# Performance work log

Measured on AMD Instinct MI355X. Metric: run time of the kernel, lower is better.

The kernel has to match this reference:

```python
import jax, jax.numpy as jnp
import numpy as np

N_HEADS = 8

def setup_inputs() -> dict:
    key = jax.random.key(0)
    k0, k1, k2, k3, k4 = jax.random.split(key, 5)
    B, S, D = 2, 2048, 1024
    scale = 0.02
    return {
        "x": jax.random.normal(k0, (B, S, D), dtype=jnp.float32),
        "Wk": jax.random.normal(k1, (D, D), dtype=jnp.float32) * scale,
        "Wv": jax.random.normal(k2, (D, D), dtype=jnp.float32) * scale,
        "Wself": jax.random.normal(k3, (D, D), dtype=jnp.float32) * scale,
        "Wout": jax.random.normal(k4, (D, D), dtype=jnp.float32) * scale,
    }

def reference(x, Wk, Wv, Wself, Wout):
    B, S, D = x.shape
    H = N_HEADS
    hd = D // H
    # torch Linear: y = x @ W.T (no bias)
    keys = (x @ Wk.T).reshape(B, S, H, hd).transpose(0, 2, 1, 3)  # [B,H,S,hd]
    vals = (x @ Wv.T).reshape(B, S, H, hd).transpose(0, 2, 1, 3)  # [B,H,S,hd]
    # energy = K K^T / sqrt(hd); weights = softmax(-energy) with causal mask
    neg_energy = -jnp.einsum("bhqd,bhkd->bhqk", keys, keys) / jnp.sqrt(
        jnp.asarray(hd, dtype=x.dtype))
    causal = jnp.tril(jnp.ones((S, S), dtype=bool))  # allowed positions
    neg_energy = jnp.where(causal, neg_energy, -jnp.inf)
    weights = jax.nn.softmax(neg_energy, axis=-1)  # [B,H,S,S]
    pairwise = jnp.einsum("bhqk,bhkd->bhqd", weights, vals)
    pairwise = pairwise.transpose(0, 2, 1, 3).reshape(B, S, D)
    self_force = x @ Wself.T
    return (pairwise + self_force) @ Wout.T
```

## Files before the change

### kernel.cpp

```cpp
#include <hip/hip_runtime.h>


typedef unsigned short u16;
typedef short s16x8 __attribute__((ext_vector_type(8)));
typedef short s16x4 __attribute__((ext_vector_type(4)));
typedef unsigned short u16x4 __attribute__((ext_vector_type(4)));
typedef unsigned short u16x8 __attribute__((ext_vector_type(8)));
typedef float f32x4 __attribute__((ext_vector_type(4)));

#define DEV __device__ __forceinline__

DEV u16 f2bf(float f) {
    union { float f; unsigned u; } v; v.f = f;
    return (u16)((v.u + 0x7FFFu + ((v.u >> 16) & 1u)) >> 16);
}
DEV float bf2f(u16 h) {
    union { unsigned u; float f; } v; v.u = ((unsigned)h) << 16;
    return v.f;
}
DEV void gload16(const void* g, void* l) {
    __builtin_amdgcn_global_load_lds(
        (const __attribute__((address_space(1))) void*)g,
        (__attribute__((address_space(3))) void*)l, 16, 0, 0);
}

#define FULL_BARRIER()                          \
    do {                                        \
        __builtin_amdgcn_sched_barrier(0);      \
        __builtin_amdgcn_s_barrier();           \
        __builtin_amdgcn_sched_barrier(0);      \
    } while (0)

__global__ __launch_bounds__(256) void cast_all(
    const float* __restrict__ x, const float* __restrict__ wk,
    const float* __restrict__ wv, const float* __restrict__ wsf,
    const float* __restrict__ wo,
    u16* __restrict__ xb, u16* __restrict__ wkb, u16* __restrict__ wvb,
    u16* __restrict__ wsb, u16* __restrict__ wob) {
    int i = blockIdx.x * 256 + threadIdx.x;
    const int NX = (2 * 2048 * 1024) / 4;
    const int NW = (1024 * 1024) / 4;
    const float* src; u16* dst; int off;
    if (i < NX)              { src = x;   dst = xb;  off = i; }
    else if (i < NX + NW)    { src = wk;  dst = wkb; off = i - NX; }
    else if (i < NX + 2*NW)  { src = wv;  dst = wvb; off = i - NX - NW; }
    else if (i < NX + 3*NW)  { src = wsf; dst = wsb; off = i - NX - 2*NW; }
    else                     { src = wo;  dst = wob; off = i - NX - 3*NW; }
    float4 v = ((const float4*)src)[off];
    u16x4 o = { f2bf(v.x), f2bf(v.y), f2bf(v.z), f2bf(v.w) };
    ((u16x4*)dst)[off] = o;
}

template <int MODE, int BN>
__global__ __launch_bounds__(256) void gemm_nt(
    const u16* __restrict__ A, const u16* __restrict__ W0,
    const u16* __restrict__ W1, const u16* __restrict__ W2,
    u16* __restrict__ O0, u16* __restrict__ O1, u16* __restrict__ O2,
    float* __restrict__ Of) {
    constexpr int NJ = BN / 32;
    constexpr int BLOADS = (BN * 64) / 4096;
    __shared__ __align__(16) u16 As[3][128 * 32];
    __shared__ __align__(16) u16 Bs[3][BN * 32];
    const int tid = threadIdx.x, lane = tid & 63, wave = tid >> 6;
    const int wr = wave >> 1, wc = wave & 1;
    const int m0 = blockIdx.y * 128, n0 = blockIdx.x * BN;
    const u16* Bw = W0;
    if (MODE == 0) Bw = (blockIdx.z == 0) ? W0 : (blockIdx.z == 1) ? W1 : W2;

    f32x4 acc[4][NJ];
#pragma unroll
    for (int i = 0; i < 4; ++i)
#pragma unroll
        for (int j = 0; j < NJ; ++j) acc[i][j] = f32x4{0.f, 0.f, 0.f, 0.f};

    const int o1 = wave * 1024 + lane * 16;
    const int r1 = o1 >> 6, c1 = (o1 & 63) >> 1;
    const int o2 = o1 + 4096;
    const int r2 = o2 >> 6, c2 = (o2 & 63) >> 1;

    auto stage = [&](int k0, int buf) {
        char* ab = (char*)As + buf * 8192;
        char* bb = (char*)Bs + buf * (BN * 64);
        gload16(A + ((size_t)(m0 + r1) << 10) + k0 + c1, ab + wave * 1024);
        gload16(A + ((size_t)(m0 + r2) << 10) + k0 + c2, ab + 4096 + wave * 1024);
        gload16(Bw + ((size_t)(n0 + r1) << 10) + k0 + c1, bb + wave * 1024);
        if constexpr (BLOADS == 2)
            gload16(Bw + ((size_t)(n0 + r2) << 10) + k0 + c2, bb + 4096 + wave * 1024);
    };

    stage(0, 0);
    stage(32, 1);
    int cur = 0;
    for (int t = 0; t < 32; ++t) {
        if (t < 31) {
            if constexpr (BLOADS == 2)
                asm volatile("s_waitcnt vmcnt(4)" ::: "memory");
            else
                asm volatile("s_waitcnt vmcnt(3)" ::: "memory");
        } else {
            asm volatile("s_waitcnt vmcnt(0)" ::: "memory");
        }
        FULL_BARRIER();
        if (t + 2 < 32) {
            int nb = cur + 2; if (nb >= 3) nb -= 3;
            stage((t + 2) << 5, nb);
        }
        const int kb = (lane >> 4) << 3;
        const u16* Ac = As[0] + cur * 4096;
        const u16* Bc = Bs[0] + cur * (BN * 32);
        s16x8 af[4], bfr[NJ];
#pragma unroll
        for (int i = 0; i < 4; ++i)
            af[i] = *(const s16x8*)&Ac[(wr * 64 + i * 16 + (lane & 15)) * 32 + kb];
#pragma unroll
        for (int j = 0; j < NJ; ++j)
            bfr[j] = *(const s16x8*)&Bc[(wc * (BN / 2) + j * 16 + (lane & 15)) * 32 + kb];
#pragma unroll
        for (int i = 0; i < 4; ++i)
#pragma unroll
            for (int j = 0; j < NJ; ++j)
                acc[i][j] = __builtin_amdgcn_mfma_f32_16x16x32_bf16(af[i], bfr[j], acc[i][j], 0, 0, 0);
        ++cur; if (cur == 3) cur = 0;
    }

    const int mb0 = m0 + wr * 64, nb0 = n0 + wc * (BN / 2);
    if (MODE == 1) {
#pragma unroll
        for (int i = 0; i < 4; ++i)
#pragma unroll
            for (int j = 0; j < NJ; ++j) {
                int n = nb0 + j * 16 + (lane & 15);
                int mbase = mb0 + i * 16 + ((lane >> 4) << 2);
#pragma unroll
                for (int r = 0; r < 4; ++r)
                    Of[((size_t)(mbase + r) << 10) + n] = acc[i][j][r];
            }
    } else if (blockIdx.z == 1) {
#pragma unroll
        for (int i = 0; i < 4; ++i)
#pragma unroll
            for (int j = 0; j < NJ; ++j) {
                int n = nb0 + j * 16 + (lane & 15);
                int h = n >> 7, d = n & 127;
                int mbase = mb0 + i * 16 + ((lane >> 4) << 2);
                int b = mbase >> 11, s = mbase & 2047;
                u16x4 pk;
#pragma unroll
                for (int r = 0; r < 4; ++r) pk[r] = f2bf(acc[i][j][r]);
                *(u16x4*)(O1 + (((size_t)(b * 8 + h) << 7) + d) * 2048 + s) = pk;
            }
    } else {
        u16* dst = blockIdx.z ? O2 : O0;
#pragma unroll
        for (int i = 0; i < 4; ++i)
#pragma unroll
            for (int j = 0; j < NJ; ++j) {
                int n = nb0 + j * 16 + (lane & 15);
                int mbase = mb0 + i * 16 + ((lane >> 4) << 2);
#pragma unroll
                for (int r = 0; r < 4; ++r)
                    dst[((size_t)(mbase + r) << 10) + n] = f2bf(acc[i][j][r]);
            }
    }
}

#define MINIT (-30000.0f)
#define MASKV (-60000.0f)
__global__ __launch_bounds__(256, 4) void attn_split(
    const u16* __restrict__ Kb, const u16* __restrict__ Vtb,
    u16* __restrict__ Op0, u16* __restrict__ Op1,
    float* __restrict__ Mp, float* __restrict__ Lp) {
    __shared__ __align__(16) u16 Ks[2][32 * 128];
    __shared__ __align__(16) u16 Vs[2][128 * 32];
    const int tid = threadIdx.x, lane = tid & 63, wave = tid >> 6;
    const int q_raw = blockIdx.x >> 1, half = blockIdx.x & 1;
    const int bh = blockIdx.y, b = bh >> 3, h = bh & 7;
    const int qt = ((bh >> 2) & 1) ? q_raw : (31 - q_raw);
    const int hi = lane >> 4, lo = lane & 15;
    const int qrow = qt * 64 + wave * 16 + lo;

    s16x8 qf[4];
    {
        const u16* qp = Kb + ((size_t)(b * 2048 + qrow) << 10) + h * 128 + (hi << 3);
#pragma unroll
        for (int c = 0; c < 4; ++c) qf[c] = *(const s16x8*)(qp + c * 32);
    }

    const u16* ksrc[2];
    const u16* vsrc[2];
    int ldst[2];
#pragma unroll
    for (int jj = 0; jj < 2; ++jj) {
        int p = wave * 2048 + jj * 1024 + lane * 16;
        ldst[jj] = wave * 2048 + jj * 1024;
        int rk = p >> 8, cbs = (p & 255) ^ ((rk & 7) << 4);
        ksrc[jj] = Kb + ((size_t)(b * 2048 + rk) << 10) + h * 128 + (cbs >> 1);
        int dv = p >> 6, kbs = (p & 63) ^ ((dv & 3) << 4);
        vsrc[jj] = Vtb + (((size_t)(bh * 128 + dv)) << 11) + (kbs >> 1);
    }
    auto stage = [&](int ks0, int buf) {
        char* kb = (char*)Ks[buf];
        char* vb = (char*)Vs[buf];
#pragma unroll
        for (int jj = 0; jj < 2; ++jj) {
            gload16(ksrc[jj] + ((size_t)ks0 << 10), kb + ldst[jj]);
            gload16(vsrc[jj] + ks0, vb + ldst[jj]);
        }
    };

    f32x4 oacc[8];
#pragma unroll
    for (int nf = 0; nf < 8; ++nf) oacc[nf] = f32x4{0.f, 0.f, 0.f, 0.f};
    float mrun = MINIT, lrun = 0.f;
    const float SC = -0.12751741566723328f;

    const int j0 = half ? (qt + 1) : 0;
    const int j1 = j0 + qt + 1;

    stage(j0 << 5, 0);
    for (int j = j0; j < j1; ++j) {
        const int cur = (j - j0) & 1;
        asm volatile("s_waitcnt vmcnt(0)" ::: "memory");
        FULL_BARRIER();
        if (j + 1 < j1) stage((j + 1) << 5, cur ^ 1);

        f32x4 sf[2];
        __builtin_amdgcn_s_setprio(1);
#pragma unroll
        for (int mf = 0; mf < 2; ++mf) {
            f32x4 s = {0.f, 0.f, 0.f, 0.f};
            int kr = mf * 16 + lo;
            const char* rowp = (const char*)Ks[cur] + kr * 256;
            int swz = (kr & 7) << 4;
#pragma unroll
            for (int c = 0; c < 4; ++c) {
                s16x8 kf = *(const s16x8*)(rowp + ((c * 64 + hi * 16) ^ swz));
                s = __builtin_amdgcn_mfma_f32_16x16x32_bf16(kf, qf[c], s, 0, 0, 0);
            }
            sf[mf] = s;
        }
        __builtin_amdgcn_s_setprio(0);

        const bool diag = (j >= 2 * qt);
        float p[2][4];
        float pm = MASKV;
#pragma unroll
        for (int mf = 0; mf < 2; ++mf)
#pragma unroll
            for (int r = 0; r < 4; ++r) {
                float sv = sf[mf][r] * SC;
                if (diag) {
                    int kg = j * 32 + mf * 16 + (hi << 2) + r;
                    if (kg > qrow) sv = MASKV;
                }
                p[mf][r] = sv;
                pm = fmaxf(pm, sv);
            }
        pm = fmaxf(pm, __shfl_xor(pm, 16));
        pm = fmaxf(pm, __shfl_xor(pm, 32));

        const bool grow = !__all(pm <= mrun);
        float mnew = mrun;
        if (grow) {
            mnew = fmaxf(mrun, pm);
            float corr = exp2f(mrun - mnew);
            lrun *= corr;
            float cr[4];
#pragma unroll
            for (int r = 0; r < 4; ++r) cr[r] = __shfl(corr, (hi << 2) + r);
#pragma unroll
            for (int nf = 0; nf < 8; ++nf)
#pragma unroll
                for (int r = 0; r < 4; ++r) oacc[nf][r] *= cr[r];
            mrun = mnew;
        }

        float psum = 0.f;
        float p2[2][4];
#pragma unroll
        for (int mf = 0; mf < 2; ++mf)
#pragma unroll
            for (int r = 0; r < 4; ++r) {
                float e = exp2f(p[mf][r] - mnew);
                p2[mf][r] = e;
                psum += e;
            }
        psum += __shfl_xor(psum, 16);
        psum += __shfl_xor(psum, 32);
        lrun += psum;

        unsigned pw0, pw1, pw2, pw3;
        asm("v_cvt_pk_bf16_f32 %0, %1, %2" : "=v"(pw0) : "v"(p2[0][0]), "v"(p2[0][1]));
        asm("v_cvt_pk_bf16_f32 %0, %1, %2" : "=v"(pw1) : "v"(p2[0][2]), "v"(p2[0][3]));
        asm("v_cvt_pk_bf16_f32 %0, %1, %2" : "=v"(pw2) : "v"(p2[1][0]), "v"(p2[1][1]));
        asm("v_cvt_pk_bf16_f32 %0, %1, %2" : "=v"(pw3) : "v"(p2[1][2]), "v"(p2[1][3]));
        union { unsigned w[4]; s16x8 v; } pau;
        pau.w[0] = pw0; pau.w[1] = pw1; pau.w[2] = pw2; pau.w[3] = pw3;
        s16x8 pa = pau.v;

        __builtin_amdgcn_s_setprio(1);
#pragma unroll
        for (int nf = 0; nf < 8; ++nf) {
            int d = nf * 16 + lo;
            const char* vrow = (const char*)Vs[cur] + d * 64;
            int swz = (d & 3) << 4;
            int ob = hi << 3;
            s16x4 vlo = *(const s16x4*)(vrow + (ob ^ swz));
            s16x4 vhi = *(const s16x4*)(vrow + ((ob + 32) ^ swz));
            s16x8 vf = {vlo[0], vlo[1], vlo[2], vlo[3], vhi[0], vhi[1], vhi[2], vhi[3]};
            oacc[nf] = __builtin_amdgcn_mfma_f32_16x16x32_bf16(pa, vf, oacc[nf], 0, 0, 0);
        }
        __builtin_amdgcn_s_setprio(0);
    }

    if (hi == 0) {
        int mi = (half * 16 + bh) * 2048 + qrow;
        Mp[mi] = mrun;
        Lp[mi] = lrun;
    }
    u16* Op = half ? Op1 : Op0;
#pragma unroll
    for (int nf = 0; nf < 8; ++nf) {
        int d = nf * 16 + lo;
#pragma unroll
        for (int r = 0; r < 4; ++r) {
            int q2 = qt * 64 + wave * 16 + (hi << 2) + r;
            Op[((size_t)(b * 2048 + q2) << 10) + h * 128 + d] = f2bf(oacc[nf][r]);
        }
    }
}

__global__ __launch_bounds__(256) void attn_combine(
    const u16* __restrict__ O0, const u16* __restrict__ O1,
    const float* __restrict__ Mp, const float* __restrict__ Lp,
    const u16* __restrict__ Sb, u16* __restrict__ Tb) {
    int i = blockIdx.x * 256 + threadIdx.x;
    int d0 = (i & 15) << 3;
    int row = i >> 4;
    int h = row & 7;
    int bq = row >> 3;
    int b = bq >> 11, q = bq & 2047;
    int bh = b * 8 + h;
    int mi0 = bh * 2048 + q, mi1 = (16 + bh) * 2048 + q;
    float m0 = Mp[mi0], m1 = Mp[mi1], l0 = Lp[mi0], l1 = Lp[mi1];
    float m = fmaxf(m0, m1);
    float a0 = exp2f(m0 - m), a1 = exp2f(m1 - m);
    float rd = 1.0f / (l0 * a0 + l1 * a1);
    size_t base = ((size_t)bq << 10) + (h << 7) + d0;
    s16x8 o0 = *(const s16x8*)(O0 + base);
    s16x8 o1 = *(const s16x8*)(O1 + base);
    s16x8 sf = *(const s16x8*)(Sb + base);
    u16x8 out;
#pragma unroll
    for (int e = 0; e < 8; ++e)
        out[e] = f2bf((bf2f((u16)o0[e]) * a0 + bf2f((u16)o1[e]) * a1) * rd + bf2f((u16)sf[e]));
    *(u16x8*)(Tb + base) = out;
}

extern "C" void kernel_launch(void* const* d_in, const int* in_sizes, int n_in,
                              void* d_out, int out_size, void* d_ws, size_t ws_size,
                              hipStream_t stream) {
    const float* x   = (const float*)d_in[0];
    const float* Wk  = (const float*)d_in[1];
    const float* Wv  = (const float*)d_in[2];
    const float* Wsf = (const float*)d_in[3];
    const float* Wo  = (const float*)d_in[4];
    float* out = (float*)d_out;
    char* ws = (char*)d_ws;
    u16* xb  = (u16*)(ws);
    u16* wkb = (u16*)(ws + (8u << 20));
    u16* wvb = (u16*)(ws + (10u << 20));
    u16* wsb = (u16*)(ws + (12u << 20));
    u16* Kb  = (u16*)(ws + (16u << 20));
    u16* Vtb = (u16*)(ws + (24u << 20));
    u16* Sbf = (u16*)(ws + (32u << 20));
    u16* Tb  = xb;

    u16* wob   = (u16*)(ws + (40u << 20));
    u16* Op0   = xb;
    u16* Op1   = (u16*)(ws + (8u << 20));
    float* Mp  = (float*)(ws + (42u << 20));
    float* Lp  = (float*)(ws + (42u << 20) + (256u << 10));

    cast_all<<<8192, 256, 0, stream>>>(x, Wk, Wv, Wsf, Wo, xb, wkb, wvb, wsb, wob);
    gemm_nt<0, 128><<<dim3(8, 32, 3), 256, 0, stream>>>(xb, wkb, wvb, wsb, Kb, Vtb, Sbf, nullptr);
    attn_split<<<dim3(64, 16), 256, 0, stream>>>(Kb, Vtb, Op0, Op1, Mp, Lp);
    attn_combine<<<2048, 256, 0, stream>>>(Op0, Op1, Mp, Lp, Sbf, Tb);
    gemm_nt<1, 64><<<dim3(16, 32, 1), 256, 0, stream>>>(Tb, wob, nullptr, nullptr,
                                                        nullptr, nullptr, nullptr, out);
}
```

Baseline: 228.1 us.

## Rewrite projection GEMMs with larger tiles, swizzled LDS and concatenated weights

Replaces the templated gemm_nt with gemm_big. It uses 256x128 (QKV-self) or 128x128 (output) block tiles, each wave owning full-width rows, and an XOR-swizzled LDS layout to reduce bank conflicts. The three input weights are cast into one contiguous buffer, so a single 2D grid covers all three projections. The pipeline drops from triple-buffered with partial waits to double-buffered with a full vmcnt(0) wait. This gives more reuse per tile and fewer conflicts, but risks exposing load latency and leaving fewer blocks to fill the CUs.

```diff
diff --git a/kernel.cpp b/kernel.cpp
--- a/kernel.cpp
+++ b/kernel.cpp
@@ -51,116 +51,113 @@
     ((u16x4*)dst)[off] = o;
 }
 
-template <int MODE, int BN>
-__global__ __launch_bounds__(256) void gemm_nt(
-    const u16* __restrict__ A, const u16* __restrict__ W0,
-    const u16* __restrict__ W1, const u16* __restrict__ W2,
-    u16* __restrict__ O0, u16* __restrict__ O1, u16* __restrict__ O2,
+template <int MODE>
+__global__ __launch_bounds__(256, 2) void gemm_big(
+    const u16* __restrict__ A, const u16* __restrict__ W,
+    u16* __restrict__ Kb, u16* __restrict__ Vtb, u16* __restrict__ Sbf,
     float* __restrict__ Of) {
-    constexpr int NJ = BN / 32;
-    constexpr int BLOADS = (BN * 64) / 4096;
-    __shared__ __align__(16) u16 As[3][128 * 32];
-    __shared__ __align__(16) u16 Bs[3][BN * 32];
+    constexpr int BM = (MODE == 0) ? 256 : 128;
+    constexpr int MF = BM / 64;
+    __shared__ __align__(16) u16 As[2][BM * 32];
+    __shared__ __align__(16) u16 Bs[2][128 * 32];
     const int tid = threadIdx.x, lane = tid & 63, wave = tid >> 6;
-    const int wr = wave >> 1, wc = wave & 1;
-    const int m0 = blockIdx.y * 128, n0 = blockIdx.x * BN;
-    const u16* Bw = W0;
-    if (MODE == 0) Bw = (blockIdx.z == 0) ? W0 : (blockIdx.z == 1) ? W1 : W2;
-
-    f32x4 acc[4][NJ];
-#pragma unroll
-    for (int i = 0; i < 4; ++i)
-#pragma unroll
-        for (int j = 0; j < NJ; ++j) acc[i][j] = f32x4{0.f, 0.f, 0.f, 0.f};
-
-    const int o1 = wave * 1024 + lane * 16;
-    const int r1 = o1 >> 6, c1 = (o1 & 63) >> 1;
-    const int o2 = o1 + 4096;
-    const int r2 = o2 >> 6, c2 = (o2 & 63) >> 1;
-
+    const int hi = lane >> 4, lo = lane & 15;
+    const int m0 = blockIdx.y * BM, n0 = blockIdx.x * 128;
+
+    f32x4 acc[MF][8];
+#pragma unroll
+    for (int i = 0; i < MF; ++i)
+#pragma unroll
+        for (int j = 0; j < 8; ++j) acc[i][j] = f32x4{0.f, 0.f, 0.f, 0.f};
+
+    const u16* asrc[MF]; int adst[MF];
+#pragma unroll
+    for (int q = 0; q < MF; ++q) {
+        int p = wave * (MF * 1024) + q * 1024 + lane * 16;
+        adst[q] = wave * (MF * 1024) + q * 1024;
+        int rw = p >> 6, cb = (p & 63) ^ (((rw >> 1) & 3) << 4);
+        asrc[q] = A + ((size_t)(m0 + rw) << 10) + (cb >> 1);
+    }
+    const u16* bsrc[2]; int bdst[2];
+#pragma unroll
+    for (int q = 0; q < 2; ++q) {
+        int p = wave * 2048 + q * 1024 + lane * 16;
+        bdst[q] = wave * 2048 + q * 1024;
+        int rw = p >> 6, cb = (p & 63) ^ (((rw >> 1) & 3) << 4);
+        bsrc[q] = W + ((size_t)(n0 + rw) << 10) + (cb >> 1);
+    }
     auto stage = [&](int k0, int buf) {
-        char* ab = (char*)As + buf * 8192;
-        char* bb = (char*)Bs + buf * (BN * 64);
-        gload16(A + ((size_t)(m0 + r1) << 10) + k0 + c1, ab + wave * 1024);
-        gload16(A + ((size_t)(m0 + r2) << 10) + k0 + c2, ab + 4096 + wave * 1024);
-        gload16(Bw + ((size_t)(n0 + r1) << 10) + k0 + c1, bb + wave * 1024);
-        if constexpr (BLOADS == 2)
-            gload16(Bw + ((size_t)(n0 + r2) << 10) + k0 + c2, bb + 4096 + wave * 1024);
+#pragma unroll
+        for (int q = 0; q < MF; ++q) gload16(asrc[q] + k0, (char*)As[buf] + adst[q]);
+#pragma unroll
+        for (int q = 0; q < 2; ++q) gload16(bsrc[q] + k0, (char*)Bs[buf] + bdst[q]);
     };
 
     stage(0, 0);
-    stage(32, 1);
-    int cur = 0;
+    const int hb = hi << 4;
     for (int t = 0; t < 32; ++t) {
-        if (t < 31) {
-            if constexpr (BLOADS == 2)
-                asm volatile("s_waitcnt vmcnt(4)" ::: "memory");
-            else
-                asm volatile("s_waitcnt vmcnt(3)" ::: "memory");
-        } else {
-            asm volatile("s_waitcnt vmcnt(0)" ::: "memory");
-        }
+        const int cur = t & 1;
+        asm volatile("s_waitcnt vmcnt(0)" ::: "memory");
         FULL_BARRIER();
-        if (t + 2 < 32) {
-            int nb = cur + 2; if (nb >= 3) nb -= 3;
-            stage((t + 2) << 5, nb);
-        }
-        const int kb = (lane >> 4) << 3;
-        const u16* Ac = As[0] + cur * 4096;
-        const u16* Bc = Bs[0] + cur * (BN * 32);
-        s16x8 af[4], bfr[NJ];
-#pragma unroll
-        for (int i = 0; i < 4; ++i)
-            af[i] = *(const s16x8*)&Ac[(wr * 64 + i * 16 + (lane & 15)) * 32 + kb];
-#pragma unroll
-        for (int j = 0; j < NJ; ++j)
-            bfr[j] = *(const s16x8*)&Bc[(wc * (BN / 2) + j * 16 + (lane & 15)) * 32 + kb];
-#pragma unroll
-        for (int i = 0; i < 4; ++i)
-#pragma unroll
-            for (int j = 0; j < NJ; ++j)
+        if (t < 31) stage((t + 1) << 5, cur ^ 1);
+        s16x8 af[MF], bfr[8];
+#pragma unroll
+        for (int i = 0; i < MF; ++i) {
+            int rw = wave * (MF * 16) + i * 16 + lo;
+            af[i] = *(const s16x8*)((const char*)As[cur] + rw * 64 + (hb ^ (((rw >> 1) & 3) << 4)));
+        }
+#pragma unroll
+        for (int j = 0; j < 8; ++j) {
+            int rw = j * 16 + lo;
+            bfr[j] = *(const s16x8*)((const char*)Bs[cur] + rw * 64 + (hb ^ (((rw >> 1) & 3) << 4)));
+        }
+#pragma unroll
+        for (int i = 0; i < MF; ++i)
+#pragma unroll
+            for (int j = 0; j < 8; ++j)
                 acc[i][j] = __builtin_amdgcn_mfma_f32_16x16x32_bf16(af[i], bfr[j], acc[i][j], 0, 0, 0);
-        ++cur; if (cur == 3) cur = 0;
-    }
-
-    const int mb0 = m0 + wr * 64, nb0 = n0 + wc * (BN / 2);
+    }
+
     if (MODE == 1) {
 #pragma unroll
-        for (int i = 0; i < 4; ++i)
-#pragma unroll
-            for (int j = 0; j < NJ; ++j) {
-                int n = nb0 + j * 16 + (lane & 15);
-                int mbase = mb0 + i * 16 + ((lane >> 4) << 2);
+        for (int i = 0; i < MF; ++i)
+#pragma unroll
+            for (int j = 0; j < 8; ++j) {
+                int n = n0 + j * 16 + lo;
+                int mbase = m0 + wave * (MF * 16) + i * 16 + (hi << 2);
 #pragma unroll
                 for (int r = 0; r < 4; ++r)
                     Of[((size_t)(mbase + r) << 10) + n] = acc[i][j][r];
             }
-    } else if (blockIdx.z == 1) {
-#pragma unroll
-        for (int i = 0; i < 4; ++i)
-#pragma unroll
-            for (int j = 0; j < NJ; ++j) {
-                int n = nb0 + j * 16 + (lane & 15);
-                int h = n >> 7, d = n & 127;
-                int mbase = mb0 + i * 16 + ((lane >> 4) << 2);
-                int b = mbase >> 11, s = mbase & 2047;
-                u16x4 pk;
-#pragma unroll
-                for (int r = 0; r < 4; ++r) pk[r] = f2bf(acc[i][j][r]);
-                *(u16x4*)(O1 + (((size_t)(b * 8 + h) << 7) + d) * 2048 + s) = pk;
-            }
     } else {
-        u16* dst = blockIdx.z ? O2 : O0;
-#pragma unroll
-        for (int i = 0; i < 4; ++i)
-#pragma unroll
-            for (int j = 0; j < NJ; ++j) {
-                int n = nb0 + j * 16 + (lane & 15);
-                int mbase = mb0 + i * 16 + ((lane >> 4) << 2);
-#pragma unroll
-                for (int r = 0; r < 4; ++r)
-                    dst[((size_t)(mbase + r) << 10) + n] = f2bf(acc[i][j][r]);
-            }
+        const int seg = n0 >> 10, nn0 = n0 & 1023;
+        if (seg == 1) {
+#pragma unroll
+            for (int i = 0; i < MF; ++i)
+#pragma unroll
+                for (int j = 0; j < 8; ++j) {
+                    int n = nn0 + j * 16 + lo;
+                    int h = n >> 7, d = n & 127;
+                    int mbase = m0 + wave * (MF * 16) + i * 16 + (hi << 2);
+                    int b = mbase >> 11, s = mbase & 2047;
+                    u16x4 pk;
+#pragma unroll
+                    for (int r = 0; r < 4; ++r) pk[r] = f2bf(acc[i][j][r]);
+                    *(u16x4*)(Vtb + (((size_t)(b * 8 + h) << 7) + d) * 2048 + s) = pk;
+                }
+        } else {
+            u16* dst = seg ? Sbf : Kb;
+#pragma unroll
+            for (int i = 0; i < MF; ++i)
+#pragma unroll
+                for (int j = 0; j < 8; ++j) {
+                    int n = nn0 + j * 16 + lo;
+                    int mbase = m0 + wave * (MF * 16) + i * 16 + (hi << 2);
+#pragma unroll
+                    for (int r = 0; r < 4; ++r)
+                        dst[((size_t)(mbase + r) << 10) + n] = f2bf(acc[i][j][r]);
+                }
+        }
     }
 }
 
@@ -367,14 +364,12 @@
     const float* Wo  = (const float*)d_in[4];
     float* out = (float*)d_out;
     char* ws = (char*)d_ws;
-    u16* xb  = (u16*)(ws);
-    u16* wkb = (u16*)(ws + (8u << 20));
-    u16* wvb = (u16*)(ws + (10u << 20));
-    u16* wsb = (u16*)(ws + (12u << 20));
-    u16* Kb  = (u16*)(ws + (16u << 20));
-    u16* Vtb = (u16*)(ws + (24u << 20));
-    u16* Sbf = (u16*)(ws + (32u << 20));
-    u16* Tb  = xb;
+    u16* xb   = (u16*)(ws);
+    u16* wcat = (u16*)(ws + (8u << 20));
+    u16* Kb   = (u16*)(ws + (16u << 20));
+    u16* Vtb  = (u16*)(ws + (24u << 20));
+    u16* Sbf  = (u16*)(ws + (32u << 20));
+    u16* Tb   = xb;
 
     u16* wob   = (u16*)(ws + (40u << 20));
     u16* Op0   = xb;
@@ -382,10 +377,10 @@
     float* Mp  = (float*)(ws + (42u << 20));
     float* Lp  = (float*)(ws + (42u << 20) + (256u << 10));
 
-    cast_all<<<8192, 256, 0, stream>>>(x, Wk, Wv, Wsf, Wo, xb, wkb, wvb, wsb, wob);
-    gemm_nt<0, 128><<<dim3(8, 32, 3), 256, 0, stream>>>(xb, wkb, wvb, wsb, Kb, Vtb, Sbf, nullptr);
+    cast_all<<<8192, 256, 0, stream>>>(x, Wk, Wv, Wsf, Wo,
+                                       xb, wcat, wcat + (1u << 20), wcat + (2u << 20), wob);
+    gemm_big<0><<<dim3(24, 16), 256, 0, stream>>>(xb, wcat, Kb, Vtb, Sbf, nullptr);
     attn_split<<<dim3(64, 16), 256, 0, stream>>>(Kb, Vtb, Op0, Op1, Mp, Lp);
     attn_combine<<<2048, 256, 0, stream>>>(Op0, Op1, Mp, Lp, Sbf, Tb);
-    gemm_nt<1, 64><<<dim3(16, 32, 1), 256, 0, stream>>>(Tb, wob, nullptr, nullptr,
-                                                        nullptr, nullptr, nullptr, out);
-}
+    gemm_big<1><<<dim3(8, 32), 256, 0, stream>>>(Tb, wob, nullptr, nullptr, nullptr, out);
+}
```

New measurement: 227.5 us. Within noise of the previous version (-0.3%).
